# Optimization experiments

Hardware: AMD Instinct MI355X
Metric: run time of the kernel (lower is better)

## Reference

```python
import jax, jax.numpy as jnp
import numpy as np

N = 100_000      # nodes
E = 1_600_000    # edges (avg degree 16)
D = 64           # node feature dim
C = 2            # num_classes
K = 2            # propagation hops


def setup_inputs() -> dict:
    key = jax.random.key(0)
    k1, k2, k3 = jax.random.split(key, 3)
    x = jax.random.normal(k1, (N, D), dtype=jnp.float32)
    edge_index = jax.random.randint(k2, (2, E), 0, N, dtype=jnp.int64)
    W = jax.random.normal(k3, (C, D), dtype=jnp.float32) * 0.1  # torch Linear weight [out,in]
    b = jnp.zeros((C,), dtype=jnp.float32)
    return {"x": x, "edge_index": edge_index, "W": W, "b": b}


def reference(x, edge_index, W, b):
    n = x.shape[0]
    self_loop = jnp.arange(n, dtype=edge_index.dtype)
    row = jnp.concatenate([edge_index[0], self_loop])  # source
    col = jnp.concatenate([edge_index[1], self_loop])  # target
    # GCN symmetric normalization with self-loops (PyG gcn_norm)
    deg = jax.ops.segment_sum(jnp.ones(col.shape, dtype=x.dtype), col, num_segments=n)
    dinv = jnp.where(deg > 0, jax.lax.rsqrt(deg), 0.0)
    norm = dinv[row] * dinv[col]                      # [E+N]
    # K-hop propagation: x <- A_hat x
    for _ in range(K):
        x = jax.ops.segment_sum(norm[:, None] * x[row], col, num_segments=n)
    logits = x @ W.T + b                               # [N, C]
    return jax.nn.log_softmax(logits, axis=1)
```

## Files before the change

### kernel.cpp

```cpp
#include <hip/hip_runtime.h>
#include <hip/hip_bf16.h>
#include <math.h>


#define NODES 100000
#define EDGES 1600000
#define DIM 64

#define PBITS 8
#define PSIZE 256
#define P_BUCKETS 391
#define CAP 8192

#define PART_BLOCKS 256
#define PART_EDGES (EDGES / PART_BLOCKS)
#define PART_PAIRS (PART_EDGES / 2)

#define PROJ_BLOCKS 782
#define NODES_PER_PROJ 128

__global__ __launch_bounds__(256) void part_kernel(const void* __restrict__ ei,
                                                   int* __restrict__ cursor,
                                                   int* __restrict__ ecbuf) {
  __shared__ int shMode;
  __shared__ int lcnt[P_BUCKETS];
  __shared__ int lbase[P_BUCKETS];
  const int t = threadIdx.x;
  if (t < 64) {
    const int* p = (const int*)ei;
    unsigned long long ball = __ballot(p[2 * t + 1] == 0);
    if (t == 0) shMode = (ball == ~0ULL) ? 1 : 0;
  }
  for (int i = t; i < P_BUCKETS; i += 256) lcnt[i] = 0;
  __syncthreads();
  const int m = shMode;
  const int pbase = blockIdx.x * PART_PAIRS;

  if (m) {
    const longlong2* cp =
        (const longlong2*)((const long long*)ei + EDGES) + pbase;
    for (int i = t; i < PART_PAIRS; i += 256) {
      longlong2 v = cp[i];
      atomicAdd(&lcnt[((int)v.x) >> PBITS], 1);
      atomicAdd(&lcnt[((int)v.y) >> PBITS], 1);
    }
  } else {
    const int2* cp = (const int2*)((const int*)ei + EDGES) + pbase;
    for (int i = t; i < PART_PAIRS; i += 256) {
      int2 v = cp[i];
      atomicAdd(&lcnt[v.x >> PBITS], 1);
      atomicAdd(&lcnt[v.y >> PBITS], 1);
    }
  }
  __syncthreads();
  for (int i = t; i < P_BUCKETS; i += 256) {
    int c = lcnt[i];
    lbase[i] = c ? atomicAdd(&cursor[i], c) : 0;
    lcnt[i] = 0;
  }
  __syncthreads();

  if (m) {
    const longlong2* rp = (const longlong2*)ei + pbase;
    const longlong2* cp =
        (const longlong2*)((const long long*)ei + EDGES) + pbase;
    for (int i = t; i < PART_PAIRS; i += 256) {
      longlong2 rv = rp[i];
      longlong2 cv = cp[i];
      {
        int r = (int)rv.x, c = (int)cv.x, bk = c >> PBITS;
        int rel = lbase[bk] + atomicAdd(&lcnt[bk], 1);
        if (rel < CAP) ecbuf[bk * CAP + rel] = (r << PBITS) | (c & (PSIZE - 1));
      }
      {
        int r = (int)rv.y, c = (int)cv.y, bk = c >> PBITS;
        int rel = lbase[bk] + atomicAdd(&lcnt[bk], 1);
        if (rel < CAP) ecbuf[bk * CAP + rel] = (r << PBITS) | (c & (PSIZE - 1));
      }
    }
  } else {
    const int2* rp = (const int2*)ei + pbase;
    const int2* cp = (const int2*)((const int*)ei + EDGES) + pbase;
    for (int i = t; i < PART_PAIRS; i += 256) {
      int2 rv = rp[i];
      int2 cv = cp[i];
      {
        int bk = cv.x >> PBITS;
        int rel = lbase[bk] + atomicAdd(&lcnt[bk], 1);
        if (rel < CAP)
          ecbuf[bk * CAP + rel] = (rv.x << PBITS) | (cv.x & (PSIZE - 1));
      }
      {
        int bk = cv.y >> PBITS;
        int rel = lbase[bk] + atomicAdd(&lcnt[bk], 1);
        if (rel < CAP)
          ecbuf[bk * CAP + rel] = (rv.y << PBITS) | (cv.y & (PSIZE - 1));
      }
    }
  }
}

__global__ __launch_bounds__(256) void degproj_kernel(
    const int* __restrict__ cursor, const int* __restrict__ ecbuf,
    const float* __restrict__ x, const float* __restrict__ W,
    float4* __restrict__ uq) {
  const int b = blockIdx.x;
  const int t = threadIdx.x;
  if (b < P_BUCKETS) {
    __shared__ int h[PSIZE];
    h[t] = 0;
    __syncthreads();
    const int cnt = min(cursor[b], CAP);
    const int* ep = ecbuf + b * CAP;
    for (int e = t; e < cnt; e += 256) atomicAdd(&h[ep[e] & (PSIZE - 1)], 1);
    __syncthreads();
    const int node = (b << PBITS) + t;
    if (node < NODES) uq[node].z = rsqrtf((float)(h[t] + 1));
  } else {
    const int nbase = (b - P_BUCKETS) * NODES_PER_PROJ;
    const int lane16 = t & 15;
    const int sub = t >> 4;
    const float4 w0 = *(const float4*)&W[lane16 * 4];
    const float4 w1 = *(const float4*)&W[DIM + lane16 * 4];
    for (int k = sub; k < NODES_PER_PROJ; k += 16) {
      const int node = nbase + k;
      if (node < NODES) {
        float4 xv = *(const float4*)&x[(size_t)node * DIM + lane16 * 4];
        float p0 = xv.x * w0.x + xv.y * w0.y + xv.z * w0.z + xv.w * w0.w;
        float p1 = xv.x * w1.x + xv.y * w1.y + xv.z * w1.z + xv.w * w1.w;
#pragma unroll
        for (int off = 8; off >= 1; off >>= 1) {
          p0 += __shfl_xor(p0, off, 16);
          p1 += __shfl_xor(p1, off, 16);
        }
        if (lane16 == 0) *(float2*)&uq[node] = make_float2(p0, p1);
      }
    }
  }
}

__global__ __launch_bounds__(256) void hop1_kernel(
    const int* __restrict__ cursor, const int* __restrict__ ecbuf,
    const float4* __restrict__ uq, float2* __restrict__ z) {
  __shared__ float ax[PSIZE];
  __shared__ float ay[PSIZE];
  const int b = blockIdx.x;
  const int t = threadIdx.x;
  ax[t] = 0.f;
  ay[t] = 0.f;
  __syncthreads();
  const int cnt = min(cursor[b], CAP);
  const int* ep = ecbuf + b * CAP;
  for (int e = t; e < cnt; e += 256) {
    int pk = ep[e];
    float4 q = uq[pk >> PBITS];
    int l = pk & (PSIZE - 1);
    atomicAdd(&ax[l], q.z * q.x);
    atomicAdd(&ay[l], q.z * q.y);
  }
  __syncthreads();
  const int node = (b << PBITS) + t;
  if (node < NODES) {
    float4 q = uq[node];
    float d = q.z;
    float s = d * d;
    z[node] = make_float2(s * (ax[t] + d * q.x), s * (ay[t] + d * q.y));
  }
}

__global__ __launch_bounds__(256) void hop2_kernel(
    const int* __restrict__ cursor, const int* __restrict__ ecbuf,
    const float2* __restrict__ z, const float4* __restrict__ uq,
    const float* __restrict__ bias, float2* __restrict__ out) {
  __shared__ float ax[PSIZE];
  __shared__ float ay[PSIZE];
  const int b = blockIdx.x;
  const int t = threadIdx.x;
  ax[t] = 0.f;
  ay[t] = 0.f;
  __syncthreads();
  const int cnt = min(cursor[b], CAP);
  const int* ep = ecbuf + b * CAP;
  for (int e = t; e < cnt; e += 256) {
    int pk = ep[e];
    float2 v = z[pk >> PBITS];
    int l = pk & (PSIZE - 1);
    atomicAdd(&ax[l], v.x);
    atomicAdd(&ay[l], v.y);
  }
  __syncthreads();
  const int node = (b << PBITS) + t;
  if (node < NODES) {
    float d = uq[node].z;
    float2 zi = z[node];
    float l0 = d * (ax[t] + zi.x) + bias[0];
    float l1 = d * (ay[t] + zi.y) + bias[1];
    float m = fmaxf(l0, l1);
    float ls = m + logf(expf(l0 - m) + expf(l1 - m));
    out[node] = make_float2(l0 - ls, l1 - ls);
  }
}

extern "C" void kernel_launch(void* const* d_in, const int* in_sizes, int n_in,
                              void* d_out, int out_size, void* d_ws,
                              size_t ws_size, hipStream_t stream) {
  const float* x = (const float*)d_in[0];
  const void* ei = d_in[1];
  const float* W = (const float*)d_in[2];
  const float* bias = (const float*)d_in[3];
  float2* out = (float2*)d_out;

  char* w = (char*)d_ws;
  size_t off = 0;
  auto alloc = [&](size_t bytes) -> char* {
    char* p = w + off;
    off += (bytes + 255) & ~(size_t)255;
    return p;
  };
  int* cursor = (int*)alloc(P_BUCKETS * sizeof(int));
  int* ecbuf = (int*)alloc((size_t)P_BUCKETS * CAP * sizeof(int));
  float4* uq = (float4*)alloc((size_t)(P_BUCKETS << PBITS) * sizeof(float4));
  float2* z = (float2*)alloc((size_t)NODES * sizeof(float2));
  (void)ws_size;

  hipMemsetAsync(cursor, 0, P_BUCKETS * sizeof(int), stream);
  part_kernel<<<PART_BLOCKS, 256, 0, stream>>>(ei, cursor, ecbuf);
  degproj_kernel<<<P_BUCKETS + PROJ_BLOCKS, 256, 0, stream>>>(cursor, ecbuf, x,
                                                              W, uq);
  hop1_kernel<<<P_BUCKETS, 256, 0, stream>>>(cursor, ecbuf, uq, z);
  hop2_kernel<<<P_BUCKETS, 256, 0, stream>>>(cursor, ecbuf, z, uq, bias, out);
}
```

Baseline: 154.2 us.

## Merge projection into partition kernel and widen bucket kernels to 1024 threads

Moves the x·W projection out of the degree kernel and into the partition kernel, so projection blocks run alongside the edge bucketing. Partition blocks are halved to 128. Degree and both hop kernels now run 1024-thread blocks that read the bucketed edge lists as int4, which gives more memory-level parallelism per bucket. The risks are more contention on the shared-memory atomics within each block and fewer partition blocks doing the bucketing.

```diff
diff --git a/kernel.cpp b/kernel.cpp
--- a/kernel.cpp
+++ b/kernel.cpp
@@ -12,112 +12,98 @@
 #define P_BUCKETS 391
 #define CAP 8192
 
-#define PART_BLOCKS 256
-#define PART_EDGES (EDGES / PART_BLOCKS)
-#define PART_PAIRS (PART_EDGES / 2)
+#define PART_BLOCKS 128
+#define PART_PAIRS (EDGES / 2 / PART_BLOCKS)
 
 #define PROJ_BLOCKS 782
 #define NODES_PER_PROJ 128
-
-__global__ __launch_bounds__(256) void part_kernel(const void* __restrict__ ei,
-                                                   int* __restrict__ cursor,
-                                                   int* __restrict__ ecbuf) {
-  __shared__ int shMode;
-  __shared__ int lcnt[P_BUCKETS];
-  __shared__ int lbase[P_BUCKETS];
-  const int t = threadIdx.x;
-  if (t < 64) {
-    const int* p = (const int*)ei;
-    unsigned long long ball = __ballot(p[2 * t + 1] == 0);
-    if (t == 0) shMode = (ball == ~0ULL) ? 1 : 0;
-  }
-  for (int i = t; i < P_BUCKETS; i += 256) lcnt[i] = 0;
-  __syncthreads();
-  const int m = shMode;
-  const int pbase = blockIdx.x * PART_PAIRS;
-
-  if (m) {
-    const longlong2* cp =
-        (const longlong2*)((const long long*)ei + EDGES) + pbase;
-    for (int i = t; i < PART_PAIRS; i += 256) {
-      longlong2 v = cp[i];
-      atomicAdd(&lcnt[((int)v.x) >> PBITS], 1);
-      atomicAdd(&lcnt[((int)v.y) >> PBITS], 1);
+#define K1_BLOCKS (PART_BLOCKS + PROJ_BLOCKS)
+
+__global__ __launch_bounds__(256) void partproj_kernel(
+    const void* __restrict__ ei, int* __restrict__ cursor,
+    int* __restrict__ ecbuf, const float* __restrict__ x,
+    const float* __restrict__ W, float4* __restrict__ uq) {
+  const int t = threadIdx.x;
+  if (blockIdx.x < PART_BLOCKS) {
+    __shared__ int shMode;
+    __shared__ int lcnt[P_BUCKETS];
+    __shared__ int lbase[P_BUCKETS];
+    if (t < 64) {
+      const int* p = (const int*)ei;
+      unsigned long long ball = __ballot(p[2 * t + 1] == 0);
+      if (t == 0) shMode = (ball == ~0ULL) ? 1 : 0;
+    }
+    for (int i = t; i < P_BUCKETS; i += 256) lcnt[i] = 0;
+    __syncthreads();
+    const int m = shMode;
+    const int pbase = blockIdx.x * PART_PAIRS;
+
+    if (m) {
+      const longlong2* cp =
+          (const longlong2*)((const long long*)ei + EDGES) + pbase;
+      for (int i = t; i < PART_PAIRS; i += 256) {
+        longlong2 v = cp[i];
+        atomicAdd(&lcnt[((int)v.x) >> PBITS], 1);
+        atomicAdd(&lcnt[((int)v.y) >> PBITS], 1);
+      }
+    } else {
+      const int2* cp = (const int2*)((const int*)ei + EDGES) + pbase;
+      for (int i = t; i < PART_PAIRS; i += 256) {
+        int2 v = cp[i];
+        atomicAdd(&lcnt[v.x >> PBITS], 1);
+        atomicAdd(&lcnt[v.y >> PBITS], 1);
+      }
+    }
+    __syncthreads();
+    for (int i = t; i < P_BUCKETS; i += 256) {
+      int c = lcnt[i];
+      lbase[i] = c ? atomicAdd(&cursor[i], c) : 0;
+      lcnt[i] = 0;
+    }
+    __syncthreads();
+
+    if (m) {
+      const longlong2* rp = (const longlong2*)ei + pbase;
+      const longlong2* cp =
+          (const longlong2*)((const long long*)ei + EDGES) + pbase;
+      for (int i = t; i < PART_PAIRS; i += 256) {
+        longlong2 rv = rp[i];
+        longlong2 cv = cp[i];
+        {
+          int r = (int)rv.x, c = (int)cv.x, bk = c >> PBITS;
+          int rel = lbase[bk] + atomicAdd(&lcnt[bk], 1);
+          if (rel < CAP)
+            ecbuf[bk * CAP + rel] = (r << PBITS) | (c & (PSIZE - 1));
+        }
+        {
+          int r = (int)rv.y, c = (int)cv.y, bk = c >> PBITS;
+          int rel = lbase[bk] + atomicAdd(&lcnt[bk], 1);
+          if (rel < CAP)
+            ecbuf[bk * CAP + rel] = (r << PBITS) | (c & (PSIZE - 1));
+        }
+      }
+    } else {
+      const int2* rp = (const int2*)ei + pbase;
+      const int2* cp = (const int2*)((const int*)ei + EDGES) + pbase;
+      for (int i = t; i < PART_PAIRS; i += 256) {
+        int2 rv = rp[i];
+        int2 cv = cp[i];
+        {
+          int bk = cv.x >> PBITS;
+          int rel = lbase[bk] + atomicAdd(&lcnt[bk], 1);
+          if (rel < CAP)
+            ecbuf[bk * CAP + rel] = (rv.x << PBITS) | (cv.x & (PSIZE - 1));
+        }
+        {
+          int bk = cv.y >> PBITS;
+          int rel = lbase[bk] + atomicAdd(&lcnt[bk], 1);
+          if (rel < CAP)
+            ecbuf[bk * CAP + rel] = (rv.y << PBITS) | (cv.y & (PSIZE - 1));
+        }
+      }
     }
   } else {
-    const int2* cp = (const int2*)((const int*)ei + EDGES) + pbase;
-    for (int i = t; i < PART_PAIRS; i += 256) {
-      int2 v = cp[i];
-      atomicAdd(&lcnt[v.x >> PBITS], 1);
-      atomicAdd(&lcnt[v.y >> PBITS], 1);
-    }
-  }
-  __syncthreads();
-  for (int i = t; i < P_BUCKETS; i += 256) {
-    int c = lcnt[i];
-    lbase[i] = c ? atomicAdd(&cursor[i], c) : 0;
-    lcnt[i] = 0;
-  }
-  __syncthreads();
-
-  if (m) {
-    const longlong2* rp = (const longlong2*)ei + pbase;
-    const longlong2* cp =
-        (const longlong2*)((const long long*)ei + EDGES) + pbase;
-    for (int i = t; i < PART_PAIRS; i += 256) {
-      longlong2 rv = rp[i];
-      longlong2 cv = cp[i];
-      {
-        int r = (int)rv.x, c = (int)cv.x, bk = c >> PBITS;
-        int rel = lbase[bk] + atomicAdd(&lcnt[bk], 1);
-        if (rel < CAP) ecbuf[bk * CAP + rel] = (r << PBITS) | (c & (PSIZE - 1));
-      }
-      {
-        int r = (int)rv.y, c = (int)cv.y, bk = c >> PBITS;
-        int rel = lbase[bk] + atomicAdd(&lcnt[bk], 1);
-        if (rel < CAP) ecbuf[bk * CAP + rel] = (r << PBITS) | (c & (PSIZE - 1));
-      }
-    }
-  } else {
-    const int2* rp = (const int2*)ei + pbase;
-    const int2* cp = (const int2*)((const int*)ei + EDGES) + pbase;
-    for (int i = t; i < PART_PAIRS; i += 256) {
-      int2 rv = rp[i];
-      int2 cv = cp[i];
-      {
-        int bk = cv.x >> PBITS;
-        int rel = lbase[bk] + atomicAdd(&lcnt[bk], 1);
-        if (rel < CAP)
-          ecbuf[bk * CAP + rel] = (rv.x << PBITS) | (cv.x & (PSIZE - 1));
-      }
-      {
-        int bk = cv.y >> PBITS;
-        int rel = lbase[bk] + atomicAdd(&lcnt[bk], 1);
-        if (rel < CAP)
-          ecbuf[bk * CAP + rel] = (rv.y << PBITS) | (cv.y & (PSIZE - 1));
-      }
-    }
-  }
-}
-
-__global__ __launch_bounds__(256) void degproj_kernel(
-    const int* __restrict__ cursor, const int* __restrict__ ecbuf,
-    const float* __restrict__ x, const float* __restrict__ W,
-    float4* __restrict__ uq) {
-  const int b = blockIdx.x;
-  const int t = threadIdx.x;
-  if (b < P_BUCKETS) {
-    __shared__ int h[PSIZE];
-    h[t] = 0;
-    __syncthreads();
-    const int cnt = min(cursor[b], CAP);
-    const int* ep = ecbuf + b * CAP;
-    for (int e = t; e < cnt; e += 256) atomicAdd(&h[ep[e] & (PSIZE - 1)], 1);
-    __syncthreads();
-    const int node = (b << PBITS) + t;
-    if (node < NODES) uq[node].z = rsqrtf((float)(h[t] + 1));
-  } else {
-    const int nbase = (b - P_BUCKETS) * NODES_PER_PROJ;
+    const int nbase = (blockIdx.x - PART_BLOCKS) * NODES_PER_PROJ;
     const int lane16 = t & 15;
     const int sub = t >> 4;
     const float4 w0 = *(const float4*)&W[lane16 * 4];
@@ -139,36 +125,72 @@
   }
 }
 
-__global__ __launch_bounds__(256) void hop1_kernel(
+__global__ __launch_bounds__(1024) void deg_kernel(
+    const int* __restrict__ cursor, const int* __restrict__ ecbuf,
+    float4* __restrict__ uq) {
+  __shared__ int h[PSIZE];
+  const int b = blockIdx.x;
+  const int t = threadIdx.x;
+  if (t < PSIZE) h[t] = 0;
+  __syncthreads();
+  const int cnt = min(cursor[b], CAP);
+  const int4* ep4 = (const int4*)(ecbuf + b * CAP);
+  for (int i = t; 4 * i < cnt; i += 1024) {
+    int4 v = ep4[i];
+    int base = 4 * i;
+    if (base + 0 < cnt) atomicAdd(&h[v.x & (PSIZE - 1)], 1);
+    if (base + 1 < cnt) atomicAdd(&h[v.y & (PSIZE - 1)], 1);
+    if (base + 2 < cnt) atomicAdd(&h[v.z & (PSIZE - 1)], 1);
+    if (base + 3 < cnt) atomicAdd(&h[v.w & (PSIZE - 1)], 1);
+  }
+  __syncthreads();
+  if (t < PSIZE) {
+    const int node = (b << PBITS) + t;
+    if (node < NODES) uq[node].z = rsqrtf((float)(h[t] + 1));
+  }
+}
+
+__global__ __launch_bounds__(1024) void hop1_kernel(
     const int* __restrict__ cursor, const int* __restrict__ ecbuf,
     const float4* __restrict__ uq, float2* __restrict__ z) {
   __shared__ float ax[PSIZE];
   __shared__ float ay[PSIZE];
   const int b = blockIdx.x;
   const int t = threadIdx.x;
-  ax[t] = 0.f;
-  ay[t] = 0.f;
+  if (t < PSIZE) {
+    ax[t] = 0.f;
+    ay[t] = 0.f;
+  }
   __syncthreads();
   const int cnt = min(cursor[b], CAP);
-  const int* ep = ecbuf + b * CAP;
-  for (int e = t; e < cnt; e += 256) {
-    int pk = ep[e];
-    float4 q = uq[pk >> PBITS];
-    int l = pk & (PSIZE - 1);
-    atomicAdd(&ax[l], q.z * q.x);
-    atomicAdd(&ay[l], q.z * q.y);
-  }
-  __syncthreads();
-  const int node = (b << PBITS) + t;
-  if (node < NODES) {
-    float4 q = uq[node];
-    float d = q.z;
-    float s = d * d;
-    z[node] = make_float2(s * (ax[t] + d * q.x), s * (ay[t] + d * q.y));
-  }
-}
-
-__global__ __launch_bounds__(256) void hop2_kernel(
+  const int4* ep4 = (const int4*)(ecbuf + b * CAP);
+  for (int i = t; 4 * i < cnt; i += 1024) {
+    int4 v = ep4[i];
+    int base = 4 * i;
+#pragma unroll
+    for (int k = 0; k < 4; k++) {
+      int pk = (k == 0) ? v.x : (k == 1) ? v.y : (k == 2) ? v.z : v.w;
+      if (base + k < cnt) {
+        float4 q = uq[pk >> PBITS];
+        int l = pk & (PSIZE - 1);
+        atomicAdd(&ax[l], q.z * q.x);
+        atomicAdd(&ay[l], q.z * q.y);
+      }
+    }
+  }
+  __syncthreads();
+  if (t < PSIZE) {
+    const int node = (b << PBITS) + t;
+    if (node < NODES) {
+      float4 q = uq[node];
+      float d = q.z;
+      float s = d * d;
+      z[node] = make_float2(s * (ax[t] + d * q.x), s * (ay[t] + d * q.y));
+    }
+  }
+}
+
+__global__ __launch_bounds__(1024) void hop2_kernel(
     const int* __restrict__ cursor, const int* __restrict__ ecbuf,
     const float2* __restrict__ z, const float4* __restrict__ uq,
     const float* __restrict__ bias, float2* __restrict__ out) {
@@ -176,28 +198,39 @@
   __shared__ float ay[PSIZE];
   const int b = blockIdx.x;
   const int t = threadIdx.x;
-  ax[t] = 0.f;
-  ay[t] = 0.f;
+  if (t < PSIZE) {
+    ax[t] = 0.f;
+    ay[t] = 0.f;
+  }
   __syncthreads();
   const int cnt = min(cursor[b], CAP);
-  const int* ep = ecbuf + b * CAP;
-  for (int e = t; e < cnt; e += 256) {
-    int pk = ep[e];
-    float2 v = z[pk >> PBITS];
-    int l = pk & (PSIZE - 1);
-    atomicAdd(&ax[l], v.x);
-    atomicAdd(&ay[l], v.y);
-  }
-  __syncthreads();
-  const int node = (b << PBITS) + t;
-  if (node < NODES) {
-    float d = uq[node].z;
-    float2 zi = z[node];
-    float l0 = d * (ax[t] + zi.x) + bias[0];
-    float l1 = d * (ay[t] + zi.y) + bias[1];
-    float m = fmaxf(l0, l1);
-    float ls = m + logf(expf(l0 - m) + expf(l1 - m));
-    out[node] = make_float2(l0 - ls, l1 - ls);
+  const int4* ep4 = (const int4*)(ecbuf + b * CAP);
+  for (int i = t; 4 * i < cnt; i += 1024) {
+    int4 v = ep4[i];
+    int base = 4 * i;
+#pragma unroll
+    for (int k = 0; k < 4; k++) {
+      int pk = (k == 0) ? v.x : (k == 1) ? v.y : (k == 2) ? v.z : v.w;
+      if (base + k < cnt) {
+        float2 zv = z[pk >> PBITS];
+        int l = pk & (PSIZE - 1);
+        atomicAdd(&ax[l], zv.x);
+        atomicAdd(&ay[l], zv.y);
+      }
+    }
+  }
+  __syncthreads();
+  if (t < PSIZE) {
+    const int node = (b << PBITS) + t;
+    if (node < NODES) {
+      float d = uq[node].z;
+      float2 zi = z[node];
+      float l0 = d * (ax[t] + zi.x) + bias[0];
+      float l1 = d * (ay[t] + zi.y) + bias[1];
+      float m = fmaxf(l0, l1);
+      float ls = m + logf(expf(l0 - m) + expf(l1 - m));
+      out[node] = make_float2(l0 - ls, l1 - ls);
+    }
   }
 }
 
@@ -224,9 +257,8 @@
   (void)ws_size;
 
   hipMemsetAsync(cursor, 0, P_BUCKETS * sizeof(int), stream);
-  part_kernel<<<PART_BLOCKS, 256, 0, stream>>>(ei, cursor, ecbuf);
-  degproj_kernel<<<P_BUCKETS + PROJ_BLOCKS, 256, 0, stream>>>(cursor, ecbuf, x,
-                                                              W, uq);
-  hop1_kernel<<<P_BUCKETS, 256, 0, stream>>>(cursor, ecbuf, uq, z);
-  hop2_kernel<<<P_BUCKETS, 256, 0, stream>>>(cursor, ecbuf, z, uq, bias, out);
-}
+  partproj_kernel<<<K1_BLOCKS, 256, 0, stream>>>(ei, cursor, ecbuf, x, W, uq);
+  deg_kernel<<<P_BUCKETS, 1024, 0, stream>>>(cursor, ecbuf, uq);
+  hop1_kernel<<<P_BUCKETS, 1024, 0, stream>>>(cursor, ecbuf, uq, z);
+  hop2_kernel<<<P_BUCKETS, 1024, 0, stream>>>(cursor, ecbuf, z, uq, bias, out);
+}
```

After: 159.5 us. +3.5%, slower.
